# Kernel tuning notes

Measured on AMD Instinct MI355X. Metric: run time of the kernel, lower is better.

The kernel has to match this reference:

```python
import jax, jax.numpy as jnp
import numpy as np

EPS = 1e-3

def layer_norm(x, w, b):
    mu = jnp.mean(x, axis=-1, keepdims=True)
    var = jnp.var(x, axis=-1, keepdims=True)
    return (x - mu) * jax.lax.rsqrt(var + EPS) * w + b

def setup_inputs() -> dict:
    key = jax.random.key(0)
    B, T, C, H = 8, 1024, 1024, 16
    Dh, F = C // H, 4 * C
    ks = jax.random.split(key, 12)
    s = 0.02
    return {
        "x":  jax.random.normal(ks[0], (B, T, C), jnp.float32),
        "Wq": jax.random.normal(ks[1], (H, C, Dh), jnp.float32) * s,
        "bq": jnp.zeros((H, Dh), jnp.float32),
        "Wk": jax.random.normal(ks[2], (H, C, Dh), jnp.float32) * s,
        "bk": jnp.zeros((H, Dh), jnp.float32),
        "Wv": jax.random.normal(ks[3], (H, C, Dh), jnp.float32) * s,
        "bv": jnp.zeros((H, Dh), jnp.float32),
        "Wp": jax.random.normal(ks[4], (C, C), jnp.float32) * s,
        "bp": jnp.zeros((C,), jnp.float32),
        "W1": jax.random.normal(ks[5], (C, F), jnp.float32) * s,
        "b1": jnp.zeros((F,), jnp.float32),
        "W2": jax.random.normal(ks[6], (F, C), jnp.float32) * s,
        "b2": jnp.zeros((C,), jnp.float32),
        "ln1_w": jnp.ones((C,), jnp.float32),
        "ln1_b": jnp.zeros((C,), jnp.float32),
        "ln2_w": jnp.ones((C,), jnp.float32),
        "ln2_b": jnp.zeros((C,), jnp.float32),
    }

def reference(x, Wq, bq, Wk, bk, Wv, bv, Wp, bp, W1, b1, W2, b2, ln1_w, ln1_b, ln2_w, ln2_b):
    B, T, C = x.shape
    # x = ln1(x); x = x + mha(x)   (residual taken from post-LN x, as in source)
    x1 = layer_norm(x, ln1_w, ln1_b)
    # all heads vectorized: q/k/v are [B, H, T, Dh]
    q = jnp.einsum('btc,hcd->bhtd', x1, Wq) + bq[:, None, :]
    k = jnp.einsum('btc,hcd->bhtd', x1, Wk) + bk[:, None, :]
    v = jnp.einsum('btc,hcd->bhtd', x1, Wv) + bv[:, None, :]
    # NOTE: source scales by full embed dim C (not head_size), and multiplies
    # the UN-softmaxed scores `wei` by v (softmax result is discarded).
    wei = jnp.einsum('bhtd,bhsd->bhts', q, k) * (C ** -0.5)
    heads = jnp.einsum('bhts,bhsd->bhtd', wei, v)            # [B,H,T,Dh]
    cat = heads.transpose(0, 2, 1, 3).reshape(B, T, C)        # concat heads
    attn = cat @ Wp + bp
    x2 = layer_norm(x1 + attn, ln2_w, ln2_b)
    h = jax.nn.gelu(x2 @ W1 + b1, approximate=False)
    return x2 + (h @ W2 + b2)
```

## Files before the change

kernel.cpp:

```cpp
#include <hip/hip_runtime.h>

typedef unsigned short u16;
typedef unsigned int u32;
typedef unsigned long long u64;
typedef __attribute__((ext_vector_type(8))) short bf16x8;
typedef __attribute__((ext_vector_type(4))) float f32x4;

__device__ __forceinline__ float b2f(u16 v) {
  union { u32 u; float f; } c; c.u = ((u32)v) << 16; return c.f;
}
__device__ __forceinline__ u16 f2b(float f) {
  union { float f; u32 u; } c; c.f = f;
  return (u16)((c.u + 0x7fffu + ((c.u >> 16) & 1u)) >> 16);
}

__device__ __forceinline__ void g2l16(const u16* g, u16* l) {
  __builtin_amdgcn_global_load_lds(
      (const __attribute__((address_space(1))) u32*)g,
      (__attribute__((address_space(3))) u32*)l,
      16, 0, 0);
}

__device__ __forceinline__ float gelu_fast(float x) {
  float z2 = -1.5957691216057308f * x * (1.0f + 0.044715f * x * x);
  z2 = fminf(fmaxf(z2, -30.f), 30.f);
  float t = __expf(z2);
  return x * __builtin_amdgcn_rcpf(1.0f + t);
}

__global__ __launch_bounds__(256)
void repack_qkv_tiled(const float* __restrict__ Wq, const float* __restrict__ Wk,
                      const float* __restrict__ Wv, u16* __restrict__ WT) {
  __shared__ u16 tile[64][65];
  const int sh = blockIdx.y, sel = sh >> 4, h = sh & 15;
  const float* W = (sel == 0) ? Wq : ((sel == 1) ? Wk : Wv);
  const int k0 = blockIdx.x * 64;
  {
    const int d = threadIdx.x & 63, r = threadIdx.x >> 6;
    #pragma unroll
    for (int i = 0; i < 16; ++i) {
      int k = r * 16 + i;
      tile[k][d] = f2b(W[(size_t)h * 65536 + (size_t)(k0 + k) * 64 + d]);
    }
  }
  __syncthreads();
  {
    const int k = threadIdx.x & 63, dd = threadIdx.x >> 6;
    #pragma unroll
    for (int i = 0; i < 16; ++i) {
      int d2 = dd * 16 + i;
      WT[((size_t)sel * 1024 + h * 64 + d2) * 1024 + k0 + k] = tile[k][d2];
    }
  }
}

__global__ __launch_bounds__(256)
void transpose_tiled(const float* __restrict__ W, u16* __restrict__ WT,
                     int N, int K) {
  __shared__ u16 tile[32][33];
  const int bx = blockIdx.x * 32;
  const int by = blockIdx.y * 32;
  const int tx = threadIdx.x & 31, ty = threadIdx.x >> 5;
  #pragma unroll
  for (int i = 0; i < 4; ++i) {
    int k = ty + i * 8;
    tile[k][tx] = f2b(W[(size_t)(by + k) * N + bx + tx]);
  }
  __syncthreads();
  #pragma unroll
  for (int i = 0; i < 4; ++i) {
    int n = ty + i * 8;
    WT[(size_t)(bx + n) * K + by + tx] = tile[tx][n];
  }
}

__global__ __launch_bounds__(256)
void ln_f32_kernel(const float* __restrict__ X, const float* __restrict__ G,
                   const float* __restrict__ Bt, u16* __restrict__ O) {
  const int row = blockIdx.x;
  const int tid = threadIdx.x;
  const float* xr = X + (size_t)row * 1024;
  float4 xv = *(const float4*)(xr + tid * 4);
  float v0 = xv.x, v1 = xv.y, v2 = xv.z, v3 = xv.w;
  float s = v0 + v1 + v2 + v3;
  float q = v0 * v0 + v1 * v1 + v2 * v2 + v3 * v3;
  #pragma unroll
  for (int off = 32; off > 0; off >>= 1) {
    s += __shfl_down(s, off);
    q += __shfl_down(q, off);
  }
  __shared__ float red[8];
  int wave = tid >> 6, lane = tid & 63;
  if (lane == 0) { red[wave] = s; red[4 + wave] = q; }
  __syncthreads();
  s = red[0] + red[1] + red[2] + red[3];
  q = red[4] + red[5] + red[6] + red[7];
  float mean = s * (1.f / 1024.f);
  float var = q * (1.f / 1024.f) - mean * mean;
  float rstd = rsqrtf(var + 1e-3f);
  float4 gv = *(const float4*)(G + tid * 4);
  float4 bv = *(const float4*)(Bt + tid * 4);
  ushort4 ov;
  ov.x = f2b((v0 - mean) * rstd * gv.x + bv.x);
  ov.y = f2b((v1 - mean) * rstd * gv.y + bv.y);
  ov.z = f2b((v2 - mean) * rstd * gv.z + bv.z);
  ov.w = f2b((v3 - mean) * rstd * gv.w + bv.w);
  *(ushort4*)(O + (size_t)row * 1024 + tid * 4) = ov;
}

__global__ __launch_bounds__(256)
void ln_bf16_kernel(const u16* __restrict__ X, const float* __restrict__ G,
                    const float* __restrict__ Bt, u16* __restrict__ O) {
  const int row = blockIdx.x;
  const int tid = threadIdx.x;
  const u16* xr = X + (size_t)row * 1024;
  ushort4 xv = *(const ushort4*)(xr + tid * 4);
  float v0 = b2f(xv.x), v1 = b2f(xv.y), v2 = b2f(xv.z), v3 = b2f(xv.w);
  float s = v0 + v1 + v2 + v3;
  float q = v0 * v0 + v1 * v1 + v2 * v2 + v3 * v3;
  #pragma unroll
  for (int off = 32; off > 0; off >>= 1) {
    s += __shfl_down(s, off);
    q += __shfl_down(q, off);
  }
  __shared__ float red[8];
  int wave = tid >> 6, lane = tid & 63;
  if (lane == 0) { red[wave] = s; red[4 + wave] = q; }
  __syncthreads();
  s = red[0] + red[1] + red[2] + red[3];
  q = red[4] + red[5] + red[6] + red[7];
  float mean = s * (1.f / 1024.f);
  float var = q * (1.f / 1024.f) - mean * mean;
  float rstd = rsqrtf(var + 1e-3f);
  float4 gv = *(const float4*)(G + tid * 4);
  float4 bv = *(const float4*)(Bt + tid * 4);
  ushort4 ov;
  ov.x = f2b((v0 - mean) * rstd * gv.x + bv.x);
  ov.y = f2b((v1 - mean) * rstd * gv.y + bv.y);
  ov.z = f2b((v2 - mean) * rstd * gv.z + bv.z);
  ov.w = f2b((v3 - mean) * rstd * gv.w + bv.w);
  *(ushort4*)(O + (size_t)row * 1024 + tid * 4) = ov;
}

template <int EPI>
__device__ __forceinline__ void gemm_epilogue(
    u16* smem, f32x4 (&acc)[4][4], void* Cout,
    const float* bias0, const float* bias1, const float* bias2,
    const u16* resid, int N, int m0, int n0,
    int tid, int wm, int wn, int quad, int l16) {
  #pragma unroll
  for (int half = 0; half < 2; ++half) {
    if (wm == half) {
      #pragma unroll
      for (int i = 0; i < 4; ++i) {
        const int fsw = (i * 4 + quad) & 7;
        #pragma unroll
        for (int j = 0; j < 4; ++j) {
          const int chunk = (wn * 8 + j * 2 + (l16 >> 3)) ^ fsw;
          const int base = chunk * 8 + (l16 & 7);
          #pragma unroll
          for (int rr = 0; rr < 4; ++rr) {
            const int lrow = i * 16 + quad * 4 + rr;
            smem[lrow * 128 + base] = f2b(acc[i][j][rr]);
          }
        }
      }
    }
    __syncthreads();
    #pragma unroll
    for (int s = 0; s < 4; ++s) {
      const int lrow = s * 16 + (tid >> 4);
      const int chunk = tid & 15;
      const int fsw = (lrow >> 2) & 7;
      bf16x8 cv = *(const bf16x8*)&smem[lrow * 128 + ((chunk ^ fsw) * 8)];
      const int gr = m0 + half * 64 + lrow;
      const int gc = n0 + chunk * 8;
      const float* bp_ = bias0;
      int cb = gc;
      if (EPI == 0) {
        const int selb = gc >> 10;
        bp_ = (selb == 0) ? bias0 : ((selb == 1) ? bias1 : bias2);
        cb = gc & 1023;
      }
      float4 bv0 = *(const float4*)(bp_ + cb);
      float4 bv1 = *(const float4*)(bp_ + cb + 4);
      float vv[8];
      #pragma unroll
      for (int e = 0; e < 8; ++e) {
        float be = (e < 4) ? ((const float*)&bv0)[e] : ((const float*)&bv1)[e - 4];
        vv[e] = b2f(((const u16*)&cv)[e]) + be;
      }
      if (EPI == 2) {
        #pragma unroll
        for (int e = 0; e < 8; ++e) vv[e] = gelu_fast(vv[e]);
      }
      if (EPI == 1 || EPI == 3) {
        bf16x8 rv = *(const bf16x8*)(resid + (size_t)gr * N + gc);
        #pragma unroll
        for (int e = 0; e < 8; ++e) vv[e] += b2f(((const u16*)&rv)[e]);
      }
      if (EPI == 3) {
        float4 o0 = {vv[0], vv[1], vv[2], vv[3]};
        float4 o1 = {vv[4], vv[5], vv[6], vv[7]};
        float* op = (float*)Cout + (size_t)gr * N + gc;
        *(float4*)op = o0;
        *(float4*)(op + 4) = o1;
      } else {
        bf16x8 ov;
        #pragma unroll
        for (int e = 0; e < 8; ++e) ((u16*)&ov)[e] = f2b(vv[e]);
        *(bf16x8*)((u16*)Cout + (size_t)gr * N + gc) = ov;
      }
    }
    __syncthreads();
  }
}

template <int EPI>
__global__ __launch_bounds__(256)
void gemm_nt2(const u16* __restrict__ A, const u16* __restrict__ BT,
              void* __restrict__ Cout,
              const float* __restrict__ bias0, const float* __restrict__ bias1,
              const float* __restrict__ bias2, const u16* __restrict__ resid,
              int M, int N, int K, int RA, int RB, int NRn) {
  __shared__ __align__(16) u16 smem[32768];
  const int tid = threadIdx.x;

  const int xcd = blockIdx.x & 7;
  const int s_ = blockIdx.x >> 3;
  const int rm = xcd / NRn, rn = xcd - rm * NRn;
  const int lm = s_ / RB, ln = s_ - lm * RB;
  const int m0 = (rm * RA + lm) * 128;
  const int n0 = (rn * RB + ln) * 128;

  const int wave = tid >> 6, lane = tid & 63;
  const int wm = wave & 1, wn = wave >> 1;
  const int quad = lane >> 4, l16 = lane & 15;

  f32x4 acc[4][4];
  #pragma unroll
  for (int i = 0; i < 4; ++i)
    #pragma unroll
    for (int j = 0; j < 4; ++j) acc[i][j] = (f32x4){0.f, 0.f, 0.f, 0.f};

  const int rowS = tid >> 3;
  const int swz = ((tid & 7) ^ ((tid >> 3) & 7)) * 8;
  const u16* aB = A + (size_t)(m0 + rowS) * K + swz;
  const u16* bB = BT + (size_t)(n0 + rowS) * K + swz;
  const size_t rstep = (size_t)32 * K;

  const int nt = K >> 6;

  auto stage = [&](int p, int kt) {
    u16* aD = &smem[(u32)p * 8192 + (u32)tid * 8];
    u16* bD = &smem[16384u + (u32)p * 8192 + (u32)tid * 8];
    const int k0 = kt * 64;
    #pragma unroll
    for (int cc = 0; cc < 4; ++cc) {
      g2l16(aB + k0 + cc * rstep, aD + cc * 2048);
      g2l16(bB + k0 + cc * rstep, bD + cc * 2048);
    }
  };

  stage(0, 0);

  for (int t = 0; t < nt; ++t) {
    const int p = t & 1;
    asm volatile("s_waitcnt vmcnt(0)" ::: "memory");
    __builtin_amdgcn_s_barrier();
    const u16* As = &smem[(u32)p * 8192];
    const u16* Bs = &smem[16384u + (u32)p * 8192];

    bf16x8 aF[2][4], bF[2][4];
    #pragma unroll
    for (int ks = 0; ks < 2; ++ks) {
      const int sOff = (((ks * 4 + quad) ^ (l16 & 7)) * 8);
      #pragma unroll
      for (int i = 0; i < 4; ++i)
        aF[ks][i] = *(const bf16x8*)&As[(wm * 64 + i * 16 + l16) * 64 + sOff];
      #pragma unroll
      for (int j = 0; j < 4; ++j)
        bF[ks][j] = *(const bf16x8*)&Bs[(wn * 64 + j * 16 + l16) * 64 + sOff];
    }
    if (t + 1 < nt) stage(p ^ 1, t + 1);
    #pragma unroll
    for (int ks = 0; ks < 2; ++ks)
      #pragma unroll
      for (int i = 0; i < 4; ++i)
        #pragma unroll
        for (int j = 0; j < 4; ++j)
          acc[i][j] = __builtin_amdgcn_mfma_f32_16x16x32_bf16(
              aF[ks][i], bF[ks][j], acc[i][j], 0, 0, 0);
  }
  __syncthreads();
  gemm_epilogue<EPI>(smem, acc, Cout, bias0, bias1, bias2, resid, N, m0, n0,
                     tid, wm, wn, quad, l16);
}

template <int EPI>
__global__ __launch_bounds__(256, 3)
void gemm_nt3(const u16* __restrict__ A, const u16* __restrict__ BT,
              void* __restrict__ Cout,
              const float* __restrict__ bias0, const float* __restrict__ bias1,
              const float* __restrict__ bias2, const u16* __restrict__ resid,
              int M, int N, int K, int RA, int RB, int NRn) {
  __shared__ __align__(16) u16 smem[24576];
  const int tid = threadIdx.x;

  const int xcd = blockIdx.x & 7;
  const int s_ = blockIdx.x >> 3;
  const int rm = xcd / NRn, rn = xcd - rm * NRn;
  const int lm = s_ / RB, ln = s_ - lm * RB;
  const int m0 = (rm * RA + lm) * 128;
  const int n0 = (rn * RB + ln) * 128;

  const int wave = tid >> 6, lane = tid & 63;
  const int wm = wave & 1, wn = wave >> 1;
  const int quad = lane >> 4, l16 = lane & 15;

  f32x4 acc[4][4];
  #pragma unroll
  for (int i = 0; i < 4; ++i)
    #pragma unroll
    for (int j = 0; j < 4; ++j) acc[i][j] = (f32x4){0.f, 0.f, 0.f, 0.f};

  const int rowS = tid >> 3;
  const int swz = ((tid & 7) ^ ((tid >> 3) & 7)) * 8;
  const u16* aB = A + (size_t)(m0 + rowS) * K + swz;
  const u16* bB = BT + (size_t)(n0 + rowS) * K + swz;
  const size_t rstep = (size_t)32 * K;

  const int nt = K >> 6;

  auto stageA = [&](int p, int kt) {
    u16* aD = &smem[(u32)p * 8192 + (u32)tid * 8];
    const int k0 = kt * 64;
    #pragma unroll
    for (int cc = 0; cc < 4; ++cc)
      g2l16(aB + k0 + cc * rstep, aD + cc * 2048);
  };
  auto stageB = [&](int kt) {
    u16* bD = &smem[16384u + (u32)tid * 8];
    const int k0 = kt * 64;
    #pragma unroll
    for (int cc = 0; cc < 4; ++cc)
      g2l16(bB + k0 + cc * rstep, bD + cc * 2048);
  };

  stageA(0, 0); stageB(0);

  for (int t = 0; t < nt; ++t) {
    const int p = t & 1;
    asm volatile("s_waitcnt vmcnt(0)" ::: "memory");
    __builtin_amdgcn_s_barrier();
    const u16* As = &smem[(u32)p * 8192];
    const u16* Bs = &smem[16384u];

    bf16x8 aF[2][4], bF[2][4];
    #pragma unroll
    for (int ks = 0; ks < 2; ++ks) {
      const int sOff = (((ks * 4 + quad) ^ (l16 & 7)) * 8);
      #pragma unroll
      for (int j = 0; j < 4; ++j)
        bF[ks][j] = *(const bf16x8*)&Bs[(wn * 64 + j * 16 + l16) * 64 + sOff];
      #pragma unroll
      for (int i = 0; i < 4; ++i)
        aF[ks][i] = *(const bf16x8*)&As[(wm * 64 + i * 16 + l16) * 64 + sOff];
    }
    asm volatile("s_waitcnt lgkmcnt(0)" ::: "memory");
    __builtin_amdgcn_s_barrier();
    if (t + 1 < nt) { stageA(p ^ 1, t + 1); stageB(t + 1); }
    #pragma unroll
    for (int ks = 0; ks < 2; ++ks)
      #pragma unroll
      for (int i = 0; i < 4; ++i)
        #pragma unroll
        for (int j = 0; j < 4; ++j)
          acc[i][j] = __builtin_amdgcn_mfma_f32_16x16x32_bf16(
              aF[ks][i], bF[ks][j], acc[i][j], 0, 0, 0);
  }
  __syncthreads();
  gemm_epilogue<EPI>(smem, acc, Cout, bias0, bias1, bias2, resid, N, m0, n0,
                     tid, wm, wn, quad, l16);
}

__global__ __launch_bounds__(256)
void attn_m_kernel(const u16* __restrict__ qkv, float* __restrict__ Mbuf) {
  const int bh = blockIdx.x;
  const int qtr = blockIdx.y;
  const int b = bh >> 4, h = bh & 15;
  const u16* Kp = qkv + (size_t)b * 1024 * 3072 + 1024 + h * 64;
  const u16* Vp = Kp + 1024 + qtr * 16;
  __shared__ __align__(16) float Ks[64 * 64];
  __shared__ __align__(16) float Vs[64 * 20];
  const int tid = threadIdx.x;
  const int d1 = tid & 63, d2q = (tid >> 6) * 4;
  const int lr = tid >> 3, lc = (tid & 7) * 8;
  const int vr = tid >> 2, vc = (tid & 3) * 4;
  float acc[4];
  #pragma unroll
  for (int j = 0; j < 4; ++j) acc[j] = 0.f;
  for (int t0 = 0; t0 < 1024; t0 += 64) {
    __syncthreads();
    #pragma unroll
    for (int it = 0; it < 2; ++it) {
      int r = it * 32 + lr;
      const u16* ks = Kp + (size_t)(t0 + r) * 3072 + lc;
      ushort4 a0 = *(const ushort4*)ks;
      ushort4 a1 = *(const ushort4*)(ks + 4);
      float* kd = &Ks[r * 64 + lc];
      kd[0] = b2f(a0.x); kd[1] = b2f(a0.y); kd[2] = b2f(a0.z); kd[3] = b2f(a0.w);
      kd[4] = b2f(a1.x); kd[5] = b2f(a1.y); kd[6] = b2f(a1.z); kd[7] = b2f(a1.w);
    }
    {
      const u16* vs = Vp + (size_t)(t0 + vr) * 3072 + vc;
      ushort4 c0 = *(const ushort4*)vs;
      float4 vvw = {b2f(c0.x), b2f(c0.y), b2f(c0.z), b2f(c0.w)};
      *(float4*)&Vs[vr * 20 + vc] = vvw;
    }
    __syncthreads();
    #pragma unroll 8
    for (int tt = 0; tt < 64; ++tt) {
      float kv = Ks[tt * 64 + d1];
      float4 vv = *(const float4*)&Vs[tt * 20 + d2q];
      #pragma unroll
      for (int j = 0; j < 4; ++j) acc[j] += kv * ((const float*)&vv)[j];
    }
  }
  float4 o = {acc[0] * 0.03125f, acc[1] * 0.03125f,
              acc[2] * 0.03125f, acc[3] * 0.03125f};
  *(float4*)(Mbuf + (size_t)bh * 4096 + d1 * 64 + qtr * 16 + d2q) = o;
}

__global__ __launch_bounds__(256)
void attn_h_kernel(const u16* __restrict__ qkv, const float* __restrict__ Mbuf,
                   u16* __restrict__ cat) {
  const int bh = blockIdx.x;
  const int tch = blockIdx.y;
  const int b = bh >> 4, h = bh & 15;
  __shared__ __align__(16) float Ms[64 * 64];
  __shared__ __align__(16) float Qs[64 * 65];
  const int tid = threadIdx.x;
  const float* Msrc = Mbuf + (size_t)bh * 4096;
  #pragma unroll
  for (int i = 0; i < 16; ++i) Ms[i * 256 + tid] = Msrc[i * 256 + tid];
  const u16* Qp = qkv + (size_t)(b * 1024 + tch * 64) * 3072 + h * 64;
  {
    const int lr = tid >> 3, lc = (tid & 7) * 8;
    #pragma unroll
    for (int it = 0; it < 2; ++it) {
      int r = it * 32 + lr;
      const u16* qs = Qp + (size_t)r * 3072 + lc;
      ushort4 a0 = *(const ushort4*)qs;
      ushort4 a1 = *(const ushort4*)(qs + 4);
      float* qd = &Qs[r * 65 + lc];
      qd[0] = b2f(a0.x); qd[1] = b2f(a0.y); qd[2] = b2f(a0.z); qd[3] = b2f(a0.w);
      qd[4] = b2f(a1.x); qd[5] = b2f(a1.y); qd[6] = b2f(a1.z); qd[7] = b2f(a1.w);
    }
  }
  __syncthreads();
  const int tl = tid >> 2, db = (tid & 3) * 16;
  float acc[16];
  #pragma unroll
  for (int j = 0; j < 16; ++j) acc[j] = 0.f;
  #pragma unroll 4
  for (int k = 0; k < 64; ++k) {
    float qv = Qs[tl * 65 + k];
    #pragma unroll
    for (int m4 = 0; m4 < 4; ++m4) {
      float4 mv = *(const float4*)&Ms[k * 64 + db + m4 * 4];
      #pragma unroll
      for (int j = 0; j < 4; ++j) acc[m4 * 4 + j] += qv * ((const float*)&mv)[j];
    }
  }
  u16* Cp = cat + (size_t)(b * 1024 + tch * 64 + tl) * 1024 + h * 64 + db;
  ushort4 o0 = {f2b(acc[0]), f2b(acc[1]), f2b(acc[2]), f2b(acc[3])};
  ushort4 o1 = {f2b(acc[4]), f2b(acc[5]), f2b(acc[6]), f2b(acc[7])};
  ushort4 o2 = {f2b(acc[8]), f2b(acc[9]), f2b(acc[10]), f2b(acc[11])};
  ushort4 o3 = {f2b(acc[12]), f2b(acc[13]), f2b(acc[14]), f2b(acc[15])};
  *(ushort4*)(Cp + 0) = o0;
  *(ushort4*)(Cp + 4) = o1;
  *(ushort4*)(Cp + 8) = o2;
  *(ushort4*)(Cp + 12) = o3;
}

extern "C" void kernel_launch(void* const* d_in, const int* in_sizes, int n_in,
                              void* d_out, int out_size, void* d_ws, size_t ws_size,
                              hipStream_t stream) {
  (void)in_sizes; (void)n_in; (void)out_size; (void)ws_size;
  const float* x     = (const float*)d_in[0];
  const float* Wq    = (const float*)d_in[1];
  const float* bq    = (const float*)d_in[2];
  const float* Wk    = (const float*)d_in[3];
  const float* bk    = (const float*)d_in[4];
  const float* Wv    = (const float*)d_in[5];
  const float* bv    = (const float*)d_in[6];
  const float* Wp    = (const float*)d_in[7];
  const float* bp    = (const float*)d_in[8];
  const float* W1    = (const float*)d_in[9];
  const float* b1    = (const float*)d_in[10];
  const float* W2    = (const float*)d_in[11];
  const float* b2    = (const float*)d_in[12];
  const float* ln1w  = (const float*)d_in[13];
  const float* ln1b  = (const float*)d_in[14];
  const float* ln2w  = (const float*)d_in[15];
  const float* ln2b  = (const float*)d_in[16];

  char* ws = (char*)d_ws;
  u16* x1    = (u16*)(ws);
  u16* qkv   = (u16*)(ws + 16777216);
  u16* cat   = (u16*)(ws + 67108864);
  u16* yb    = (u16*)(ws + 83886080);
  u16* x2    = (u16*)(ws + 100663296);
  u16* WqkvT = (u16*)(ws + 117440512);
  u16* WpT   = (u16*)(ws + 123731968);
  u16* W1T   = (u16*)(ws + 125829120);
  u16* W2T   = (u16*)(ws + 134217728);
  float* Mb  = (float*)(ws + 142606336);
  u16* hb    = (u16*)(ws + 16777216);

  repack_qkv_tiled<<<dim3(16, 48), 256, 0, stream>>>(Wq, Wk, Wv, WqkvT);
  transpose_tiled<<<dim3(32, 32), 256, 0, stream>>>(Wp, WpT, 1024, 1024);
  transpose_tiled<<<dim3(128, 32), 256, 0, stream>>>(W1, W1T, 4096, 1024);
  transpose_tiled<<<dim3(32, 128), 256, 0, stream>>>(W2, W2T, 1024, 4096);

  ln_f32_kernel<<<8192, 256, 0, stream>>>(x, ln1w, ln1b, x1);

  gemm_nt3<0><<<1536, 256, 0, stream>>>(x1, WqkvT, qkv, bq, bk, bv, nullptr,
                                        8192, 3072, 1024, 16, 12, 2);
  attn_m_kernel<<<dim3(128, 4), 256, 0, stream>>>(qkv, Mb);
  attn_h_kernel<<<dim3(128, 16), 256, 0, stream>>>(qkv, Mb, cat);

  gemm_nt2<1><<<512, 256, 0, stream>>>(cat, WpT, yb, bp, nullptr, nullptr, x1,
                                       8192, 1024, 1024, 8, 8, 1);
  ln_bf16_kernel<<<8192, 256, 0, stream>>>(yb, ln2w, ln2b, x2);

  gemm_nt3<2><<<2048, 256, 0, stream>>>(x2, W1T, hb, b1, nullptr, nullptr, nullptr,
                                        8192, 4096, 1024, 16, 16, 2);
  gemm_nt2<3><<<512, 256, 0, stream>>>(hb, W2T, d_out, b2, nullptr, nullptr, x2,
                                       8192, 1024, 4096, 8, 8, 1);
}
```

Before: 442.1 us.

## Compute attention head output with bf16 MFMA using hi/lo split of M

```diff
diff --git a/kernel.cpp b/kernel.cpp
--- a/kernel.cpp
+++ b/kernel.cpp
@@ -385,7 +385,8 @@
 }
 
 __global__ __launch_bounds__(256)
-void attn_m_kernel(const u16* __restrict__ qkv, float* __restrict__ Mbuf) {
+void attn_m_kernel(const u16* __restrict__ qkv, u16* __restrict__ MT1,
+                   u16* __restrict__ MT2) {
   const int bh = blockIdx.x;
   const int qtr = blockIdx.y;
   const int b = bh >> 4, h = bh & 15;
@@ -427,61 +428,101 @@
       for (int j = 0; j < 4; ++j) acc[j] += kv * ((const float*)&vv)[j];
     }
   }
-  float4 o = {acc[0] * 0.03125f, acc[1] * 0.03125f,
-              acc[2] * 0.03125f, acc[3] * 0.03125f};
-  *(float4*)(Mbuf + (size_t)bh * 4096 + d1 * 64 + qtr * 16 + d2q) = o;
-}
-
-__global__ __launch_bounds__(256)
-void attn_h_kernel(const u16* __restrict__ qkv, const float* __restrict__ Mbuf,
-                   u16* __restrict__ cat) {
+  #pragma unroll
+  for (int j = 0; j < 4; ++j) {
+    float m = acc[j] * 0.03125f;
+    u16 hi = f2b(m);
+    u16 lo = f2b(m - b2f(hi));
+    const size_t off = (size_t)bh * 4096 + (qtr * 16 + d2q + j) * 64 + d1;
+    MT1[off] = hi;
+    MT2[off] = lo;
+  }
+}
+
+__global__ __launch_bounds__(256)
+void attn_h_mfma(const u16* __restrict__ qkv, const u16* __restrict__ MT1,
+                 const u16* __restrict__ MT2, u16* __restrict__ cat) {
   const int bh = blockIdx.x;
-  const int tch = blockIdx.y;
+  const int tq = blockIdx.y;
   const int b = bh >> 4, h = bh & 15;
-  __shared__ __align__(16) float Ms[64 * 64];
-  __shared__ __align__(16) float Qs[64 * 65];
+  __shared__ __align__(16) u16 smem[24576];
+  u16* Qs = smem;
+  u16* Ms1 = smem + 16384;
+  u16* Ms2 = smem + 20480;
   const int tid = threadIdx.x;
-  const float* Msrc = Mbuf + (size_t)bh * 4096;
-  #pragma unroll
-  for (int i = 0; i < 16; ++i) Ms[i * 256 + tid] = Msrc[i * 256 + tid];
-  const u16* Qp = qkv + (size_t)(b * 1024 + tch * 64) * 3072 + h * 64;
+  const int wv = tid >> 6, lane = tid & 63;
+  const int quad = lane >> 4, l16 = lane & 15;
+
+  const int rowS = tid >> 3;
+  const int swz = ((tid & 7) ^ (rowS & 7)) * 8;
   {
-    const int lr = tid >> 3, lc = (tid & 7) * 8;
-    #pragma unroll
-    for (int it = 0; it < 2; ++it) {
-      int r = it * 32 + lr;
-      const u16* qs = Qp + (size_t)r * 3072 + lc;
-      ushort4 a0 = *(const ushort4*)qs;
-      ushort4 a1 = *(const ushort4*)(qs + 4);
-      float* qd = &Qs[r * 65 + lc];
-      qd[0] = b2f(a0.x); qd[1] = b2f(a0.y); qd[2] = b2f(a0.z); qd[3] = b2f(a0.w);
-      qd[4] = b2f(a1.x); qd[5] = b2f(a1.y); qd[6] = b2f(a1.z); qd[7] = b2f(a1.w);
-    }
-  }
-  __syncthreads();
-  const int tl = tid >> 2, db = (tid & 3) * 16;
-  float acc[16];
-  #pragma unroll
-  for (int j = 0; j < 16; ++j) acc[j] = 0.f;
-  #pragma unroll 4
-  for (int k = 0; k < 64; ++k) {
-    float qv = Qs[tl * 65 + k];
-    #pragma unroll
-    for (int m4 = 0; m4 < 4; ++m4) {
-      float4 mv = *(const float4*)&Ms[k * 64 + db + m4 * 4];
-      #pragma unroll
-      for (int j = 0; j < 4; ++j) acc[m4 * 4 + j] += qv * ((const float*)&mv)[j];
-    }
-  }
-  u16* Cp = cat + (size_t)(b * 1024 + tch * 64 + tl) * 1024 + h * 64 + db;
-  ushort4 o0 = {f2b(acc[0]), f2b(acc[1]), f2b(acc[2]), f2b(acc[3])};
-  ushort4 o1 = {f2b(acc[4]), f2b(acc[5]), f2b(acc[6]), f2b(acc[7])};
-  ushort4 o2 = {f2b(acc[8]), f2b(acc[9]), f2b(acc[10]), f2b(acc[11])};
-  ushort4 o3 = {f2b(acc[12]), f2b(acc[13]), f2b(acc[14]), f2b(acc[15])};
-  *(ushort4*)(Cp + 0) = o0;
-  *(ushort4*)(Cp + 4) = o1;
-  *(ushort4*)(Cp + 8) = o2;
-  *(ushort4*)(Cp + 12) = o3;
+    const u16* Qg = qkv + (size_t)(b * 1024 + tq * 256 + rowS) * 3072 +
+                    h * 64 + swz;
+    u16* qD = &Qs[(u32)tid * 8];
+    #pragma unroll
+    for (int cc = 0; cc < 8; ++cc)
+      g2l16(Qg + (size_t)cc * 32 * 3072, qD + cc * 2048);
+    const size_t moff = (size_t)bh * 4096 + rowS * 64 + swz;
+    g2l16(MT1 + moff, &Ms1[(u32)tid * 8]);
+    g2l16(MT1 + moff + 2048, &Ms1[(u32)tid * 8 + 2048]);
+    g2l16(MT2 + moff, &Ms2[(u32)tid * 8]);
+    g2l16(MT2 + moff + 2048, &Ms2[(u32)tid * 8 + 2048]);
+  }
+  asm volatile("s_waitcnt vmcnt(0)" ::: "memory");
+  __syncthreads();
+
+  f32x4 acc[4][4];
+  #pragma unroll
+  for (int i = 0; i < 4; ++i)
+    #pragma unroll
+    for (int j = 0; j < 4; ++j) acc[i][j] = (f32x4){0.f, 0.f, 0.f, 0.f};
+
+  bf16x8 aF[2][4], b1F[2][4], b2F[2][4];
+  #pragma unroll
+  for (int ks = 0; ks < 2; ++ks) {
+    const int sOff = (((ks * 4 + quad) ^ (l16 & 7)) * 8);
+    #pragma unroll
+    for (int i = 0; i < 4; ++i)
+      aF[ks][i] = *(const bf16x8*)&Qs[(wv * 64 + i * 16 + l16) * 64 + sOff];
+    #pragma unroll
+    for (int j = 0; j < 4; ++j) {
+      b1F[ks][j] = *(const bf16x8*)&Ms1[(j * 16 + l16) * 64 + sOff];
+      b2F[ks][j] = *(const bf16x8*)&Ms2[(j * 16 + l16) * 64 + sOff];
+    }
+  }
+  #pragma unroll
+  for (int ks = 0; ks < 2; ++ks)
+    #pragma unroll
+    for (int i = 0; i < 4; ++i)
+      #pragma unroll
+      for (int j = 0; j < 4; ++j) {
+        acc[i][j] = __builtin_amdgcn_mfma_f32_16x16x32_bf16(
+            aF[ks][i], b1F[ks][j], acc[i][j], 0, 0, 0);
+        acc[i][j] = __builtin_amdgcn_mfma_f32_16x16x32_bf16(
+            aF[ks][i], b2F[ks][j], acc[i][j], 0, 0, 0);
+      }
+  __syncthreads();
+
+  {
+    u16* eS = smem + wv * 4608;
+    #pragma unroll
+    for (int i = 0; i < 4; ++i)
+      #pragma unroll
+      for (int j = 0; j < 4; ++j)
+        #pragma unroll
+        for (int rr = 0; rr < 4; ++rr)
+          eS[(i * 16 + quad * 4 + rr) * 72 + j * 16 + l16] =
+              f2b(acc[i][j][rr]);
+  }
+  __syncthreads();
+  const int bT = b * 1024 + tq * 256;
+  #pragma unroll
+  for (int s = 0; s < 8; ++s) {
+    const int g = s * 32 + (tid >> 3);
+    bf16x8 v = *(const bf16x8*)&smem[(g >> 6) * 4608 + (g & 63) * 72 +
+                                     (tid & 7) * 8];
+    *(bf16x8*)(cat + (size_t)(bT + g) * 1024 + h * 64 + (tid & 7) * 8) = v;
+  }
 }
 
 extern "C" void kernel_launch(void* const* d_in, const int* in_sizes, int n_in,
@@ -516,7 +557,8 @@
   u16* WpT   = (u16*)(ws + 123731968);
   u16* W1T   = (u16*)(ws + 125829120);
   u16* W2T   = (u16*)(ws + 134217728);
-  float* Mb  = (float*)(ws + 142606336);
+  u16* MT1   = (u16*)(ws + 142606336);
+  u16* MT2   = (u16*)(ws + 143654912);
   u16* hb    = (u16*)(ws + 16777216);
 
   repack_qkv_tiled<<<dim3(16, 48), 256, 0, stream>>>(Wq, Wk, Wv, WqkvT);
@@ -528,8 +570,8 @@
 
   gemm_nt3<0><<<1536, 256, 0, stream>>>(x1, WqkvT, qkv, bq, bk, bv, nullptr,
                                         8192, 3072, 1024, 16, 12, 2);
-  attn_m_kernel<<<dim3(128, 4), 256, 0, stream>>>(qkv, Mb);
-  attn_h_kernel<<<dim3(128, 16), 256, 0, stream>>>(qkv, Mb, cat);
+  attn_m_kernel<<<dim3(128, 4), 256, 0, stream>>>(qkv, MT1, MT2);
+  attn_h_mfma<<<dim3(128, 4), 256, 0, stream>>>(qkv, MT1, MT2, cat);
 
   gemm_nt2<1><<<512, 256, 0, stream>>>(cat, WpT, yb, bp, nullptr, nullptr, x1,
                                        8192, 1024, 1024, 8, 8, 1);
```

New measurement: 441.6 us, median of 2. No clear change (-0.1%).
